# Optimization experiments

Measured on AMD Instinct MI355X. Metric: run time of the kernel, lower is better.

## Reference

```python
import jax, jax.numpy as jnp
import numpy as np

B, N, E = 8, 2000, 32000
LAT, STY, NF = 128, 64, 10
HEADS, HID = 4, 128
OUT = 3 + NF  # 13
EPS = 1e-5
SLOPE = 0.2


def _lin(k, fi, fo):
    return jax.random.normal(k, (fi, fo), dtype=jnp.float32) / np.sqrt(fi)


def setup_inputs() -> dict:
    key = jax.random.key(0)
    ks = jax.random.split(key, 32)
    inp = {
        'z': jax.random.normal(ks[0], (B, LAT), dtype=jnp.float32),
        'template_x': jax.random.normal(ks[1], (N, NF), dtype=jnp.float32),
        'template_edge_index': jax.random.randint(ks[2], (2, E), 0, N, dtype=jnp.int32),
        # style MLP
        'mlp_w1': _lin(ks[3], LAT, 256), 'mlp_b1': jnp.zeros((256,), jnp.float32),
        'mlp_w2': _lin(ks[4], 256, 512), 'mlp_b2': jnp.zeros((512,), jnp.float32),
        'mlp_w3': _lin(ks[5], 512, STY), 'mlp_b3': jnp.zeros((STY,), jnp.float32),
        # GAT1: in = NF + STY = 74 -> heads*HID = 512, concat
        'gat1_w': _lin(ks[6], NF + STY, HEADS * HID),
        'gat1_as': jax.random.normal(ks[7], (HEADS, HID), jnp.float32) * 0.1,
        'gat1_ad': jax.random.normal(ks[8], (HEADS, HID), jnp.float32) * 0.1,
        'gat1_b': jnp.zeros((HEADS * HID,), jnp.float32),
        'ln1_g': jnp.ones((HEADS * HID,), jnp.float32), 'ln1_b': jnp.zeros((HEADS * HID,), jnp.float32),
        # GAT2: 512 -> 512, concat
        'gat2_w': _lin(ks[9], HEADS * HID, HEADS * HID),
        'gat2_as': jax.random.normal(ks[10], (HEADS, HID), jnp.float32) * 0.1,
        'gat2_ad': jax.random.normal(ks[11], (HEADS, HID), jnp.float32) * 0.1,
        'gat2_b': jnp.zeros((HEADS * HID,), jnp.float32),
        'ln2_g': jnp.ones((HEADS * HID,), jnp.float32), 'ln2_b': jnp.zeros((HEADS * HID,), jnp.float32),
        # GAT3: 512 -> 13, 1 head, no concat
        'gat3_w': _lin(ks[12], HEADS * HID, OUT),
        'gat3_as': jax.random.normal(ks[13], (1, OUT), jnp.float32) * 0.1,
        'gat3_ad': jax.random.normal(ks[14], (1, OUT), jnp.float32) * 0.1,
        'gat3_b': jnp.zeros((OUT,), jnp.float32),
    }
    return inp


def gat_conv(x, src, dst, n_nodes, W, a_src, a_dst, bias, heads, out_ch, concat):
    # x: [NT, F_in]; per-head linear transform
    h = (x @ W).reshape(-1, heads, out_ch)              # [NT, H, C]
    als = jnp.sum(h * a_src[None], axis=-1)             # [NT, H]
    ald = jnp.sum(h * a_dst[None], axis=-1)             # [NT, H]
    logits = jax.nn.leaky_relu(als[src] + ald[dst], SLOPE)   # [E, H]
    # segment softmax over destination nodes (self-loops guarantee nonempty segments)
    mx = jax.ops.segment_max(logits, dst, num_segments=n_nodes)
    alpha = jnp.exp(logits - mx[dst])
    den = jax.ops.segment_sum(alpha, dst, num_segments=n_nodes)
    alpha = alpha / den[dst]                             # [E, H]
    msgs = h[src] * alpha[:, :, None]                    # [E, H, C]
    out = jax.ops.segment_sum(msgs, dst, num_segments=n_nodes)  # [NT, H, C]
    if concat:
        return out.reshape(n_nodes, heads * out_ch) + bias
    return out.mean(axis=1) + bias


def layer_norm(x, g, b):
    mu = jnp.mean(x, axis=-1, keepdims=True)
    var = jnp.mean((x - mu) ** 2, axis=-1, keepdims=True)
    return (x - mu) * jax.lax.rsqrt(var + EPS) * g + b


def reference(z, template_x, template_edge_index,
              mlp_w1, mlp_b1, mlp_w2, mlp_b2, mlp_w3, mlp_b3,
              gat1_w, gat1_as, gat1_ad, gat1_b, ln1_g, ln1_b,
              gat2_w, gat2_as, gat2_ad, gat2_b, ln2_g, ln2_b,
              gat3_w, gat3_as, gat3_ad, gat3_b):
    bsz = z.shape[0]
    n = template_x.shape[0]
    nt = bsz * n
    # batch the template graph: replicate nodes, offset edge indices per graph
    x = jnp.tile(template_x, (bsz, 1))                                  # [NT, NF]
    off = (jnp.arange(bsz, dtype=template_edge_index.dtype) * n)
    ei = (template_edge_index[:, None, :] + off[None, :, None]).reshape(2, -1)  # [2, B*E]
    loops = jnp.arange(nt, dtype=ei.dtype)
    src = jnp.concatenate([ei[0], loops])
    dst = jnp.concatenate([ei[1], loops])
    # style MLP
    s = jax.nn.leaky_relu(z @ mlp_w1 + mlp_b1, SLOPE)
    s = jax.nn.leaky_relu(s @ mlp_w2 + mlp_b2, SLOPE)
    s = s @ mlp_w3 + mlp_b3                                             # [B, STY]
    s_exp = jnp.repeat(s, n, axis=0)                                    # [NT, STY]
    H0 = jnp.concatenate([x, s_exp], axis=1)
    H1 = jax.nn.leaky_relu(gat_conv(H0, src, dst, nt, gat1_w, gat1_as, gat1_ad, gat1_b, HEADS, HID, True), SLOPE)
    H1n = layer_norm(H1, ln1_g, ln1_b)
    H2 = jax.nn.leaky_relu(gat_conv(H1n, src, dst, nt, gat2_w, gat2_as, gat2_ad, gat2_b, HEADS, HID, True), SLOPE)
    H2 = H2 + H1n
    H2n = layer_norm(H2, ln2_g, ln2_b)
    H_out = gat_conv(H2n, src, dst, nt, gat3_w, gat3_as, gat3_ad, gat3_b, 1, OUT, False)  # [NT, 13]
    delta_p = H_out[:, :3]
    delta_f = H_out[:, 3:]
    p_gen = x[:, :3] + delta_p
    X_gen = jnp.concatenate([p_gen, x[:, 3:] + delta_f[:, 3:]], axis=1)  # X[:, :3] overwritten by p_gen
    EF = p_gen[ei[1]] - p_gen[ei[0]]                                     # edge displacement vectors [B*E, 3]
    return X_gen, p_gen, EF
```

## Files before the change

kernel.cpp:

```cpp
#include <hip/hip_runtime.h>
#include <hip/hip_fp16.h>

constexpr int Bz = 8, Nn = 2000, Ee = 32000, NTOT = 16000;
constexpr int XG_OFF = 0, PG_OFF = 160000, EF_OFF = 208000;
#define SLOPE 0.2f
#define EPSL 1e-5f

typedef __attribute__((ext_vector_type(8))) _Float16 f16x8;
typedef __attribute__((ext_vector_type(4))) float float4v;

__device__ __forceinline__ float lrelu(float x) { return x > 0.f ? x : SLOPE * x; }

__device__ __forceinline__ unsigned short f2h(float x) {
  _Float16 hh = (_Float16)x;
  return *(unsigned short*)&hh;
}

__device__ __forceinline__ float wave_max(float v) {
  for (int o = 32; o; o >>= 1) v = fmaxf(v, __shfl_xor(v, o));
  return v;
}
__device__ __forceinline__ float wave_sum(float v) {
  for (int o = 32; o; o >>= 1) v += __shfl_xor(v, o);
  return v;
}

__global__ void hist_k(const int* __restrict__ tei, int* __restrict__ counts) {
  int j = blockIdx.x * 256 + threadIdx.x;
  if (j < Ee) atomicAdd(&counts[tei[Ee + j]], 1);
}

__global__ void scan_k(const int* __restrict__ counts, int* __restrict__ offs) {
  __shared__ int part[256];
  int t = threadIdx.x;
  int loc[8];
  int s = 0;
  for (int i = 0; i < 8; i++) {
    int idx = t * 8 + i;
    int c = (idx < Nn) ? counts[idx] : 0;
    loc[i] = s; s += c;
  }
  part[t] = s;
  __syncthreads();
  for (int o = 1; o < 256; o <<= 1) {
    int v = (t >= o) ? part[t - o] : 0;
    __syncthreads();
    part[t] += v;
    __syncthreads();
  }
  int excl = (t == 0) ? 0 : part[t - 1];
  for (int i = 0; i < 8; i++) {
    int idx = t * 8 + i;
    if (idx < Nn) offs[idx] = excl + loc[i];
  }
  if (t == 255) offs[Nn] = part[255];
}

__global__ void place_k(const int* __restrict__ tei, const int* __restrict__ offs,
                        int* __restrict__ cursor, int* __restrict__ colb) {
  int j = blockIdx.x * 256 + threadIdx.x;
  if (j < Ee) {
    int d = tei[Ee + j];
    int slot = offs[d] + atomicAdd(&cursor[d], 1);
    colb[slot] = tei[j];
  }
}

template <int K, int ACT>
__global__ __launch_bounds__(256) void lin_k(const float* __restrict__ x, const float* __restrict__ w,
                                             const float* __restrict__ bias, float* __restrict__ y,
                                             int O) {
  int gw = blockIdx.x * 4 + (threadIdx.x >> 6);
  int lane = threadIdx.x & 63;
  int bb = gw / O, o = gw - bb * O;
  float acc = 0.f;
#pragma unroll
  for (int k = lane; k < K; k += 64) acc += x[bb * K + k] * w[k * O + o];
  acc = wave_sum(acc);
  if (lane == 0) {
    if (bias) acc += bias[o];
    y[gw] = ACT ? lrelu(acc) : acc;
  }
}

__global__ __launch_bounds__(256) void w2bf_k(const float* __restrict__ W, unsigned short* __restrict__ Bt) {
  __shared__ float tile[32][33];
  int tx = threadIdx.x & 31, ty = threadIdx.x >> 5;
  int x0 = blockIdx.x * 32;
  int y0 = blockIdx.y * 32;
  for (int r = ty; r < 32; r += 8) tile[r][tx] = W[(y0 + r) * 512 + x0 + tx];
  __syncthreads();
  for (int r = ty; r < 32; r += 8) Bt[(x0 + r) * 512 + (y0 + tx)] = f2h(tile[tx][r]);
}

__global__ void w3t_k(const float* __restrict__ W, unsigned short* __restrict__ W3t) {
  for (int idx = threadIdx.x; idx < 8192; idx += 256) {
    int col = idx >> 9, k = idx & 511;
    float v = (col < 13) ? W[k * 13 + col] : 0.f;
    W3t[idx] = f2h(v);
  }
}

__global__ __launch_bounds__(256) void h1_k(const float* __restrict__ tx, const float* __restrict__ g1w,
                                            const float* __restrict__ pb,
                                            const float* __restrict__ a_s, const float* __restrict__ a_d,
                                            unsigned short* __restrict__ h1, float* __restrict__ als,
                                            float* __restrict__ ald) {
  int blk = blockIdx.x;
  int b = blk & 7, nl = blk >> 3;
  int n = b * Nn + nl;
  int head = threadIdx.x >> 6, lane = threadIdx.x & 63;
  int c = head * 128 + 2 * lane;
  float t0 = 0.f, t1 = 0.f;
#pragma unroll
  for (int k = 0; k < 10; k++) {
    float xv = tx[nl * 10 + k];
    float2 wv = *(const float2*)&g1w[k * 512 + c];
    t0 += xv * wv.x; t1 += xv * wv.y;
  }
  float2 pv = *(const float2*)&pb[b * 512 + c];
  float hx = t0 + pv.x, hy = t1 + pv.y;
  ushort2 st; st.x = f2h(hx); st.y = f2h(hy);
  *(ushort2*)&h1[(size_t)n * 512 + c] = st;
  float2 av = *(const float2*)&a_s[c];
  float2 dv = *(const float2*)&a_d[c];
  float pa = wave_sum(hx * av.x + hy * av.y);
  float pd = wave_sum(hx * dv.x + hy * dv.y);
  if (lane == 0) { als[n * 4 + head] = pa; ald[n * 4 + head] = pd; }
}

template <int RESID>
__global__ __launch_bounds__(256) void agg_k(const unsigned short* __restrict__ h,
                                             const float* __restrict__ als, const float* __restrict__ ald,
                                             const float* __restrict__ bias,
                                             const float* __restrict__ g, const float* __restrict__ beta,
                                             const unsigned short* __restrict__ resid,
                                             unsigned short* __restrict__ out,
                                             const int* __restrict__ offs, const int* __restrict__ colb) {
  int blk = blockIdx.x;
  int b = blk & 7, nl = blk >> 3;
  int n = b * Nn + nl;
  int w = threadIdx.x >> 6, lane = threadIdx.x & 63;
  int li = lane & 15, eg = lane >> 4;
  int rs = offs[nl];
  int nit = offs[nl + 1] - rs + 1;
  float aldn = ald[n * 4 + w];

  __shared__ float fin[512];
  __shared__ float red[8];
  __shared__ float bcs[2];

  __half2 acc2[4];
#pragma unroll
  for (int j = 0; j < 4; j++) acc2[j] = __float2half2_rn(0.f);
  float inv;
  const unsigned short* hbase = h + (size_t)(w * 128 + li * 8);

  if (nit <= 64) {
    int sg = n;
    float logit = -3e38f;
    if (lane < nit) {
      sg = (lane < nit - 1) ? colb[rs + lane] + b * Nn : n;
      logit = lrelu(als[sg * 4 + w] + aldn);
    }
    float m = wave_max(logit);
    float raw = (lane < nit) ? __expf(logit - m) : 0.f;
    inv = 1.f / wave_sum(raw);
    __half2 a2r = __float2half2_rn(raw);
    int au = *(int*)&a2r;
    for (int e = eg; e < nit; e += 4) {
      int aeu = __shfl(au, e);
      int sge = __shfl(sg, e);
      __half2 a2 = *(__half2*)&aeu;
      uint4 hv = *(const uint4*)(hbase + (size_t)sge * 512);
      acc2[0] = __hfma2(a2, *(__half2*)&hv.x, acc2[0]);
      acc2[1] = __hfma2(a2, *(__half2*)&hv.y, acc2[1]);
      acc2[2] = __hfma2(a2, *(__half2*)&hv.z, acc2[2]);
      acc2[3] = __hfma2(a2, *(__half2*)&hv.w, acc2[3]);
    }
  } else {
    float m = -3e38f;
    for (int i = lane; i < nit; i += 64) {
      int sg = (i < nit - 1) ? colb[rs + i] + b * Nn : n;
      m = fmaxf(m, lrelu(als[sg * 4 + w] + aldn));
    }
    m = wave_max(m);
    float den = 0.f;
    for (int base = 0; base < nit; base += 64) {
      int cnt = min(64, nit - base);
      int sg = n;
      float raw = 0.f;
      if (lane < cnt) {
        int i = base + lane;
        sg = (i < nit - 1) ? colb[rs + i] + b * Nn : n;
        raw = __expf(lrelu(als[sg * 4 + w] + aldn) - m);
      }
      den += raw;
      __half2 a2r = __float2half2_rn(raw);
      int au = *(int*)&a2r;
      for (int e = eg; e < cnt; e += 4) {
        int aeu = __shfl(au, e);
        int sge = __shfl(sg, e);
        __half2 a2 = *(__half2*)&aeu;
        uint4 hv = *(const uint4*)(hbase + (size_t)sge * 512);
        acc2[0] = __hfma2(a2, *(__half2*)&hv.x, acc2[0]);
        acc2[1] = __hfma2(a2, *(__half2*)&hv.y, acc2[1]);
        acc2[2] = __hfma2(a2, *(__half2*)&hv.z, acc2[2]);
        acc2[3] = __hfma2(a2, *(__half2*)&hv.w, acc2[3]);
      }
    }
    inv = 1.f / wave_sum(den);
  }

  float fv[8];
#pragma unroll
  for (int j = 0; j < 4; j++) {
    float2 f2 = __half22float2(acc2[j]);
    fv[2 * j] = f2.x; fv[2 * j + 1] = f2.y;
  }
#pragma unroll
  for (int j = 0; j < 8; j++) {
    fv[j] += __shfl_xor(fv[j], 16);
    fv[j] += __shfl_xor(fv[j], 32);
  }
  if (eg == 0) {
#pragma unroll
    for (int j = 0; j < 8; j++) fin[w * 128 + li * 8 + j] = fv[j] * inv;
  }
  __syncthreads();

  int c = 2 * threadIdx.x;
  float v0 = lrelu(fin[c] + bias[c]);
  float v1 = lrelu(fin[c + 1] + bias[c + 1]);
  if (RESID) {
    unsigned int rv = *(const unsigned int*)&resid[(size_t)n * 512 + c];
    __half2 rh = *(__half2*)&rv;
    float2 rf = __half22float2(rh);
    v0 += rf.x; v1 += rf.y;
  }
  float p1 = wave_sum(v0 + v1);
  float p2 = wave_sum(v0 * v0 + v1 * v1);
  if (lane == 0) { red[w] = p1; red[4 + w] = p2; }
  __syncthreads();
  if (threadIdx.x == 0) {
    float s1 = red[0] + red[1] + red[2] + red[3];
    float s2 = red[4] + red[5] + red[6] + red[7];
    float mu = s1 * (1.f / 512.f);
    float var = s2 * (1.f / 512.f) - mu * mu;
    bcs[0] = mu;
    bcs[1] = rsqrtf(var + EPSL);
  }
  __syncthreads();
  float mu = bcs[0], rstd = bcs[1];
  float o0 = (v0 - mu) * rstd * g[c] + beta[c];
  float o1 = (v1 - mu) * rstd * g[c + 1] + beta[c + 1];
  ushort2 st; st.x = f2h(o0); st.y = f2h(o1);
  *(ushort2*)&out[(size_t)n * 512 + c] = st;
}

__global__ __launch_bounds__(256) void gemm2_k(const unsigned short* __restrict__ A,
                                               const unsigned short* __restrict__ Bt,
                                               unsigned short* __restrict__ C,
                                               const float* __restrict__ As, const float* __restrict__ Ad,
                                               float* __restrict__ als2, float* __restrict__ ald2) {
  __shared__ char smem[32768];
  char* sAc = smem;
  char* sBc = smem + 16384;
  int t = threadIdx.x;
  int lane = t & 63, w = t >> 6;
  int wr = w >> 1, wc = w & 1;
  int m0 = blockIdx.y * 128, n0 = blockIdx.x * 128;
  int head = blockIdx.x;

  float4v acc[4][4];
#pragma unroll
  for (int i = 0; i < 4; i++)
#pragma unroll
    for (int j = 0; j < 4; j++) acc[i][j] = (float4v){0.f, 0.f, 0.f, 0.f};

  int srow[4], sklin[4], ssw[4];
#pragma unroll
  for (int i = 0; i < 4; i++) {
    int slot = i * 256 + t;
    srow[i] = slot >> 3;
    sklin[i] = (slot & 7) * 16;
    ssw[i] = srow[i] * 128 + (sklin[i] ^ ((srow[i] & 7) << 4));
  }

  uint4 va[4], vb[4];
#pragma unroll
  for (int i = 0; i < 4; i++) {
    va[i] = *(const uint4*)((const char*)A + (size_t)(m0 + srow[i]) * 1024 + sklin[i]);
    vb[i] = *(const uint4*)((const char*)Bt + (size_t)(n0 + srow[i]) * 1024 + sklin[i]);
  }

  int r_a = wr * 64 + (lane & 15);
  int r_b = wc * 64 + (lane & 15);
  int kbb = (lane >> 4) * 16;
  int sw_a = (r_a & 7) << 4;
  int sw_b = (r_b & 7) << 4;

  for (int k0 = 0; k0 < 512; k0 += 64) {
    if (k0) __syncthreads();
#pragma unroll
    for (int i = 0; i < 4; i++) {
      *(uint4*)(sAc + ssw[i]) = va[i];
      *(uint4*)(sBc + ssw[i]) = vb[i];
    }
    __syncthreads();
    if (k0 + 64 < 512) {
#pragma unroll
      for (int i = 0; i < 4; i++) {
        va[i] = *(const uint4*)((const char*)A + (size_t)(m0 + srow[i]) * 1024 + (k0 + 64) * 2 + sklin[i]);
        vb[i] = *(const uint4*)((const char*)Bt + (size_t)(n0 + srow[i]) * 1024 + (k0 + 64) * 2 + sklin[i]);
      }
    }
#pragma unroll
    for (int ksub = 0; ksub < 2; ksub++) {
      f16x8 af[4], bg[4];
#pragma unroll
      for (int m = 0; m < 4; m++)
        af[m] = *(const f16x8*)(sAc + (r_a + m * 16) * 128 + ((ksub * 64 + kbb) ^ sw_a));
#pragma unroll
      for (int nn = 0; nn < 4; nn++)
        bg[nn] = *(const f16x8*)(sBc + (r_b + nn * 16) * 128 + ((ksub * 64 + kbb) ^ sw_b));
#pragma unroll
      for (int m = 0; m < 4; m++)
#pragma unroll
        for (int nn = 0; nn < 4; nn++)
          acc[m][nn] = __builtin_amdgcn_mfma_f32_16x16x32_f16(af[m], bg[nn], acc[m][nn], 0, 0, 0);
    }
  }

  int orow = m0 + wr * 64 + (lane >> 4) * 4;
  int ocol = n0 + wc * 64 + (lane & 15);
#pragma unroll
  for (int m = 0; m < 4; m++)
#pragma unroll
    for (int nn = 0; nn < 4; nn++)
#pragma unroll
      for (int r = 0; r < 4; r++)
        C[(size_t)(orow + m * 16 + r) * 512 + ocol + nn * 16] = f2h(acc[m][nn][r]);

  __syncthreads();
  float* sRed = (float*)smem;
  int cidx0 = wc * 64 + (lane & 15);
  float asv[4], adv[4];
#pragma unroll
  for (int nn = 0; nn < 4; nn++) {
    asv[nn] = As[head * 128 + cidx0 + nn * 16];
    adv[nn] = Ad[head * 128 + cidx0 + nn * 16];
  }
#pragma unroll
  for (int m = 0; m < 4; m++) {
#pragma unroll
    for (int r = 0; r < 4; r++) {
      float pa = 0.f, pd = 0.f;
#pragma unroll
      for (int nn = 0; nn < 4; nn++) { pa += acc[m][nn][r] * asv[nn]; pd += acc[m][nn][r] * adv[nn]; }
      for (int o = 1; o < 16; o <<= 1) { pa += __shfl_xor(pa, o); pd += __shfl_xor(pd, o); }
      if ((lane & 15) == 0) {
        int rblk = wr * 64 + (lane >> 4) * 4 + m * 16 + r;
        sRed[rblk * 2 + wc] = pa;
        sRed[256 + rblk * 2 + wc] = pd;
      }
    }
  }
  __syncthreads();
  if (t < 128) {
    als2[(m0 + t) * 4 + head] = sRed[t * 2] + sRed[t * 2 + 1];
  } else {
    int r2 = t - 128;
    ald2[(m0 + r2) * 4 + head] = sRed[256 + r2 * 2] + sRed[256 + r2 * 2 + 1];
  }
}

__global__ __launch_bounds__(256) void gemm3_k(const unsigned short* __restrict__ H,
                                               const unsigned short* __restrict__ W3t,
                                               const float* __restrict__ as3, const float* __restrict__ ad3,
                                               float* __restrict__ h3, float* __restrict__ als3,
                                               float* __restrict__ ald3) {
  int w = threadIdx.x >> 6, l = threadIdx.x & 63;
  int m0 = blockIdx.x * 64 + w * 16;
  int r16 = l & 15, g4 = l >> 4;
  float4v acc = (float4v){0.f, 0.f, 0.f, 0.f};
  const unsigned short* ha = H + (size_t)(m0 + r16) * 512 + g4 * 8;
  const unsigned short* wb = W3t + (size_t)r16 * 512 + g4 * 8;
#pragma unroll
  for (int kk = 0; kk < 16; kk++) {
    f16x8 a = *(const f16x8*)(ha + kk * 32);
    f16x8 bfr = *(const f16x8*)(wb + kk * 32);
    acc = __builtin_amdgcn_mfma_f32_16x16x32_f16(a, bfr, acc, 0, 0, 0);
  }
  int col = r16;
  float asv = (col < 13) ? as3[col] : 0.f;
  float adv = (col < 13) ? ad3[col] : 0.f;
#pragma unroll
  for (int r = 0; r < 4; r++) {
    float v = acc[r];
    int row = m0 + g4 * 4 + r;
    if (col < 13) h3[row * 13 + col] = v;
    float sa = v * asv, sd = v * adv;
    for (int o = 1; o < 16; o <<= 1) { sa += __shfl_xor(sa, o); sd += __shfl_xor(sd, o); }
    if (col == 0) { als3[row] = sa; ald3[row] = sd; }
  }
}

__global__ __launch_bounds__(64) void agg3_k(const float* __restrict__ h3, const float* __restrict__ als3,
                                             const float* __restrict__ ald3, const float* __restrict__ b3,
                                             const float* __restrict__ tx, const int* __restrict__ offs,
                                             const int* __restrict__ colb, float* __restrict__ dout) {
  int blk = blockIdx.x, lane = threadIdx.x;
  int b = blk & 7, nl = blk >> 3;
  int n = b * Nn + nl;
  int rs = offs[nl], deg = offs[nl + 1] - rs;
  float aldn = ald3[n];
  float sl = lrelu(als3[n] + aldn);
  float a = 0.f, inv;
  if (deg <= 64) {
    int sgl = 0; float logit = -1e30f;
    if (lane < deg) { sgl = colb[rs + lane] + b * Nn; logit = lrelu(als3[sgl] + aldn); }
    float m = wave_max(fmaxf(logit, sl));
    float raw = (lane < deg) ? __expf(logit - m) : 0.f;
    float es = __expf(sl - m);
    inv = 1.f / (wave_sum(raw) + es);
    if (lane < 13) a = es * h3[n * 13 + lane];
    for (int e = 0; e < deg; e++) {
      float w = __shfl(raw, e);
      int sg = __shfl(sgl, e);
      if (lane < 13) a += w * h3[sg * 13 + lane];
    }
  } else {
    float m = sl;
    for (int e = lane; e < deg; e += 64) {
      int sg = colb[rs + e] + b * Nn;
      m = fmaxf(m, lrelu(als3[sg] + aldn));
    }
    m = wave_max(m);
    float es = __expf(sl - m);
    float den = (lane == 0) ? es : 0.f;
    if (lane < 13) a = es * h3[n * 13 + lane];
    for (int base = 0; base < deg; base += 64) {
      int cnt = min(64, deg - base);
      int sgl = 0; float raw = 0.f;
      if (lane < cnt) {
        sgl = colb[rs + base + lane] + b * Nn;
        raw = __expf(lrelu(als3[sgl] + aldn) - m);
      }
      den += raw;
      for (int e = 0; e < cnt; e++) {
        float w = __shfl(raw, e);
        int sg = __shfl(sgl, e);
        if (lane < 13) a += w * h3[sg * 13 + lane];
      }
    }
    inv = 1.f / wave_sum(den);
  }
  a *= inv;
  float hv = a + ((lane < 13) ? b3[lane] : 0.f);
  float txv = (lane < 10) ? tx[nl * 10 + lane] : 0.f;
  float pv = txv + hv;
  if (lane < 3) dout[PG_OFF + n * 3 + lane] = pv;
  float up = __shfl(hv, lane + 3);
  float xg = (lane < 3) ? pv : (txv + up);
  if (lane < 10) dout[XG_OFF + n * 10 + lane] = xg;
}

__global__ void ef_k(const int* __restrict__ tei, float* __restrict__ dout) {
  int e = blockIdx.x * 256 + threadIdx.x;
  int b = e / Ee, j = e - b * Ee;
  int sg = tei[j] + b * Nn;
  int dg = tei[Ee + j] + b * Nn;
  const float* pg = dout + PG_OFF;
  dout[EF_OFF + e * 3 + 0] = pg[dg * 3 + 0] - pg[sg * 3 + 0];
  dout[EF_OFF + e * 3 + 1] = pg[dg * 3 + 1] - pg[sg * 3 + 1];
  dout[EF_OFF + e * 3 + 2] = pg[dg * 3 + 2] - pg[sg * 3 + 2];
}

extern "C" void kernel_launch(void* const* d_in, const int* in_sizes, int n_in,
                              void* d_out, int out_size, void* d_ws, size_t ws_size,
                              hipStream_t stream) {
  const float* z = (const float*)d_in[0];
  const float* tx = (const float*)d_in[1];
  const int* tei = (const int*)d_in[2];
  const float* w1 = (const float*)d_in[3];
  const float* b1 = (const float*)d_in[4];
  const float* w2 = (const float*)d_in[5];
  const float* b2 = (const float*)d_in[6];
  const float* w3 = (const float*)d_in[7];
  const float* b3 = (const float*)d_in[8];
  const float* g1w = (const float*)d_in[9];
  const float* g1as = (const float*)d_in[10];
  const float* g1ad = (const float*)d_in[11];
  const float* g1b = (const float*)d_in[12];
  const float* ln1g = (const float*)d_in[13];
  const float* ln1b = (const float*)d_in[14];
  const float* g2w = (const float*)d_in[15];
  const float* g2as = (const float*)d_in[16];
  const float* g2ad = (const float*)d_in[17];
  const float* g2b = (const float*)d_in[18];
  const float* ln2g = (const float*)d_in[19];
  const float* ln2b = (const float*)d_in[20];
  const float* g3w = (const float*)d_in[21];
  const float* g3as = (const float*)d_in[22];
  const float* g3ad = (const float*)d_in[23];
  const float* g3b = (const float*)d_in[24];
  float* out = (float*)d_out;

  float* F = (float*)d_ws;
  float* pb_ = F + 0;
  float* l1_ = F + 8192;
  float* l2_ = F + 16384;
  float* s_ = F + 24576;
  float* als1 = F + 100000;
  float* ald1 = F + 164000;
  float* als2 = F + 228000;
  float* ald2 = F + 292000;
  float* als3 = F + 356000;
  float* ald3 = F + 372000;
  float* h3_ = F + 388000;
  unsigned short* U = (unsigned short*)(F + 600000);
  unsigned short* hA = U;
  unsigned short* hB = U + 8192000;
  unsigned short* Bt = U + 16384000;
  unsigned short* W3t = U + 16646144;
  int* I = (int*)(F + 10000000);
  int* counts = I;
  int* cursor = I + 2000;
  int* offs = I + 4000;
  int* colb = I + 6001;

  hipMemsetAsync(counts, 0, 4000 * sizeof(int), stream);
  hist_k<<<125, 256, 0, stream>>>(tei, counts);
  scan_k<<<1, 256, 0, stream>>>(counts, offs);
  place_k<<<125, 256, 0, stream>>>(tei, offs, cursor, colb);

  w2bf_k<<<dim3(16, 16), 256, 0, stream>>>(g2w, Bt);
  w3t_k<<<1, 256, 0, stream>>>(g3w, W3t);

  lin_k<128, 1><<<512, 256, 0, stream>>>(z, w1, b1, l1_, 256);
  lin_k<256, 1><<<1024, 256, 0, stream>>>(l1_, w2, b2, l2_, 512);
  lin_k<512, 0><<<128, 256, 0, stream>>>(l2_, w3, b3, s_, 64);
  lin_k<64, 0><<<1024, 256, 0, stream>>>(s_, g1w + 10 * 512, nullptr, pb_, 512);

  h1_k<<<NTOT, 256, 0, stream>>>(tx, g1w, pb_, g1as, g1ad, hA, als1, ald1);
  agg_k<0><<<NTOT, 256, 0, stream>>>(hA, als1, ald1, g1b, ln1g, ln1b, nullptr, hB, offs, colb);

  gemm2_k<<<dim3(4, 125), 256, 0, stream>>>(hB, Bt, hA, g2as, g2ad, als2, ald2);
  agg_k<1><<<NTOT, 256, 0, stream>>>(hA, als2, ald2, g2b, ln2g, ln2b, hB, hB, offs, colb);

  gemm3_k<<<250, 256, 0, stream>>>(hB, W3t, g3as, g3ad, h3_, als3, ald3);
  agg3_k<<<NTOT, 64, 0, stream>>>(h3_, als3, ald3, g3b, tx, offs, colb, out);
  ef_k<<<1000, 256, 0, stream>>>(tei, out);
}
```

Measured before the change: 235.2 us.

## Restructure GAT aggregation edge split and stage GEMM output through LDS

The aggregation kernel now splits edges across the four waves, with each lane covering 8 of the 512 features of a gathered row. Attention weights and source indices go through shared memory instead of wave shuffles, and per-wave partial sums are reduced in LDS before bias, residual and layernorm. This replaces 16-byte gathers from scattered lanes with full-row coalesced 1 KB reads, but adds block barriers and extra LDS traffic. The GEMM epilogue now stages its fp16 tile in padded shared memory and writes it out as 16-byte stores, replacing scattered 2-byte global stores.

```diff
diff --git a/kernel.cpp b/kernel.cpp
--- a/kernel.cpp
+++ b/kernel.cpp
@@ -141,20 +141,23 @@
   int b = blk & 7, nl = blk >> 3;
   int n = b * Nn + nl;
   int w = threadIdx.x >> 6, lane = threadIdx.x & 63;
-  int li = lane & 15, eg = lane >> 4;
   int rs = offs[nl];
   int nit = offs[nl + 1] - rs + 1;
   float aldn = ald[n * 4 + w];
 
-  __shared__ float fin[512];
+  __shared__ unsigned int alpha_u[4][68];
+  __shared__ int sgn[64];
+  __shared__ float part[4][512];
+  __shared__ float invs[4];
   __shared__ float red[8];
   __shared__ float bcs[2];
 
   __half2 acc2[4];
 #pragma unroll
   for (int j = 0; j < 4; j++) acc2[j] = __float2half2_rn(0.f);
-  float inv;
-  const unsigned short* hbase = h + (size_t)(w * 128 + li * 8);
+
+  const unsigned short* hbase = h + lane * 8;
+  int hd = lane >> 4;
 
   if (nit <= 64) {
     int sg = n;
@@ -162,21 +165,43 @@
     if (lane < nit) {
       sg = (lane < nit - 1) ? colb[rs + lane] + b * Nn : n;
       logit = lrelu(als[sg * 4 + w] + aldn);
+      if (w == 0) sgn[lane] = sg;
     }
     float m = wave_max(logit);
     float raw = (lane < nit) ? __expf(logit - m) : 0.f;
-    inv = 1.f / wave_sum(raw);
-    __half2 a2r = __float2half2_rn(raw);
-    int au = *(int*)&a2r;
-    for (int e = eg; e < nit; e += 4) {
-      int aeu = __shfl(au, e);
-      int sge = __shfl(sg, e);
-      __half2 a2 = *(__half2*)&aeu;
-      uint4 hv = *(const uint4*)(hbase + (size_t)sge * 512);
-      acc2[0] = __hfma2(a2, *(__half2*)&hv.x, acc2[0]);
-      acc2[1] = __hfma2(a2, *(__half2*)&hv.y, acc2[1]);
-      acc2[2] = __hfma2(a2, *(__half2*)&hv.z, acc2[2]);
-      acc2[3] = __hfma2(a2, *(__half2*)&hv.w, acc2[3]);
+    float den = wave_sum(raw);
+    if (lane == 0) invs[w] = 1.f / den;
+    __half2 a2 = __float2half2_rn(raw);
+    alpha_u[w][lane] = *(unsigned int*)&a2;
+    __syncthreads();
+    int e = w;
+    for (; e + 4 < nit; e += 8) {
+      unsigned int au0 = alpha_u[hd][e];
+      int sg0 = sgn[e];
+      unsigned int au1 = alpha_u[hd][e + 4];
+      int sg1 = sgn[e + 4];
+      uint4 hv0 = *(const uint4*)(hbase + (size_t)sg0 * 512);
+      uint4 hv1 = *(const uint4*)(hbase + (size_t)sg1 * 512);
+      __half2 a0 = *(__half2*)&au0;
+      __half2 a1 = *(__half2*)&au1;
+      acc2[0] = __hfma2(a0, *(__half2*)&hv0.x, acc2[0]);
+      acc2[1] = __hfma2(a0, *(__half2*)&hv0.y, acc2[1]);
+      acc2[2] = __hfma2(a0, *(__half2*)&hv0.z, acc2[2]);
+      acc2[3] = __hfma2(a0, *(__half2*)&hv0.w, acc2[3]);
+      acc2[0] = __hfma2(a1, *(__half2*)&hv1.x, acc2[0]);
+      acc2[1] = __hfma2(a1, *(__half2*)&hv1.y, acc2[1]);
+      acc2[2] = __hfma2(a1, *(__half2*)&hv1.z, acc2[2]);
+      acc2[3] = __hfma2(a1, *(__half2*)&hv1.w, acc2[3]);
+    }
+    if (e < nit) {
+      unsigned int au0 = alpha_u[hd][e];
+      int sg0 = sgn[e];
+      uint4 hv0 = *(const uint4*)(hbase + (size_t)sg0 * 512);
+      __half2 a0 = *(__half2*)&au0;
+      acc2[0] = __hfma2(a0, *(__half2*)&hv0.x, acc2[0]);
+      acc2[1] = __hfma2(a0, *(__half2*)&hv0.y, acc2[1]);
+      acc2[2] = __hfma2(a0, *(__half2*)&hv0.z, acc2[2]);
+      acc2[3] = __hfma2(a0, *(__half2*)&hv0.w, acc2[3]);
     }
   } else {
     float m = -3e38f;
@@ -194,22 +219,26 @@
         int i = base + lane;
         sg = (i < nit - 1) ? colb[rs + i] + b * Nn : n;
         raw = __expf(lrelu(als[sg * 4 + w] + aldn) - m);
+        if (w == 0) sgn[lane] = sg;
       }
       den += raw;
-      __half2 a2r = __float2half2_rn(raw);
-      int au = *(int*)&a2r;
-      for (int e = eg; e < cnt; e += 4) {
-        int aeu = __shfl(au, e);
-        int sge = __shfl(sg, e);
-        __half2 a2 = *(__half2*)&aeu;
+      __half2 a2 = __float2half2_rn(raw);
+      alpha_u[w][lane] = *(unsigned int*)&a2;
+      __syncthreads();
+      for (int e = w; e < cnt; e += 4) {
+        unsigned int au = alpha_u[hd][e];
+        int sge = sgn[e];
         uint4 hv = *(const uint4*)(hbase + (size_t)sge * 512);
-        acc2[0] = __hfma2(a2, *(__half2*)&hv.x, acc2[0]);
-        acc2[1] = __hfma2(a2, *(__half2*)&hv.y, acc2[1]);
-        acc2[2] = __hfma2(a2, *(__half2*)&hv.z, acc2[2]);
-        acc2[3] = __hfma2(a2, *(__half2*)&hv.w, acc2[3]);
+        __half2 a2e = *(__half2*)&au;
+        acc2[0] = __hfma2(a2e, *(__half2*)&hv.x, acc2[0]);
+        acc2[1] = __hfma2(a2e, *(__half2*)&hv.y, acc2[1]);
+        acc2[2] = __hfma2(a2e, *(__half2*)&hv.z, acc2[2]);
+        acc2[3] = __hfma2(a2e, *(__half2*)&hv.w, acc2[3]);
       }
-    }
-    inv = 1.f / wave_sum(den);
+      __syncthreads();
+    }
+    den = wave_sum(den);
+    if (lane == 0) invs[w] = 1.f / den;
   }
 
   float fv[8];
@@ -218,20 +247,16 @@
     float2 f2 = __half22float2(acc2[j]);
     fv[2 * j] = f2.x; fv[2 * j + 1] = f2.y;
   }
-#pragma unroll
-  for (int j = 0; j < 8; j++) {
-    fv[j] += __shfl_xor(fv[j], 16);
-    fv[j] += __shfl_xor(fv[j], 32);
-  }
-  if (eg == 0) {
-#pragma unroll
-    for (int j = 0; j < 8; j++) fin[w * 128 + li * 8 + j] = fv[j] * inv;
-  }
-  __syncthreads();
-
-  int c = 2 * threadIdx.x;
-  float v0 = lrelu(fin[c] + bias[c]);
-  float v1 = lrelu(fin[c + 1] + bias[c + 1]);
+  *(float4*)&part[w][lane * 8] = make_float4(fv[0], fv[1], fv[2], fv[3]);
+  *(float4*)&part[w][lane * 8 + 4] = make_float4(fv[4], fv[5], fv[6], fv[7]);
+  __syncthreads();
+
+  int c = 2 * (int)threadIdx.x;
+  float inv = invs[c >> 7];
+  float s0 = part[0][c] + part[1][c] + part[2][c] + part[3][c];
+  float s1 = part[0][c + 1] + part[1][c + 1] + part[2][c + 1] + part[3][c + 1];
+  float v0 = lrelu(s0 * inv + bias[c]);
+  float v1 = lrelu(s1 * inv + bias[c + 1]);
   if (RESID) {
     unsigned int rv = *(const unsigned int*)&resid[(size_t)n * 512 + c];
     __half2 rh = *(__half2*)&rv;
@@ -243,10 +268,10 @@
   if (lane == 0) { red[w] = p1; red[4 + w] = p2; }
   __syncthreads();
   if (threadIdx.x == 0) {
-    float s1 = red[0] + red[1] + red[2] + red[3];
-    float s2 = red[4] + red[5] + red[6] + red[7];
-    float mu = s1 * (1.f / 512.f);
-    float var = s2 * (1.f / 512.f) - mu * mu;
+    float s1r = red[0] + red[1] + red[2] + red[3];
+    float s2r = red[4] + red[5] + red[6] + red[7];
+    float mu = s1r * (1.f / 512.f);
+    float var = s2r * (1.f / 512.f) - mu * mu;
     bcs[0] = mu;
     bcs[1] = rsqrtf(var + EPSL);
   }
@@ -263,7 +288,7 @@
                                                unsigned short* __restrict__ C,
                                                const float* __restrict__ As, const float* __restrict__ Ad,
                                                float* __restrict__ als2, float* __restrict__ ald2) {
-  __shared__ char smem[32768];
+  __shared__ char smem[34816];
   char* sAc = smem;
   char* sBc = smem + 16384;
   int t = threadIdx.x;
@@ -332,15 +357,25 @@
     }
   }
 
-  int orow = m0 + wr * 64 + (lane >> 4) * 4;
-  int ocol = n0 + wc * 64 + (lane & 15);
+  __syncthreads();
+  unsigned short* sC = (unsigned short*)smem;
+  int rbase = wr * 64 + (lane >> 4) * 4;
+  int cbase = wc * 64 + (lane & 15);
 #pragma unroll
   for (int m = 0; m < 4; m++)
 #pragma unroll
     for (int nn = 0; nn < 4; nn++)
 #pragma unroll
       for (int r = 0; r < 4; r++)
-        C[(size_t)(orow + m * 16 + r) * 512 + ocol + nn * 16] = f2h(acc[m][nn][r]);
+        sC[(rbase + m * 16 + r) * 136 + cbase + nn * 16] = f2h(acc[m][nn][r]);
+  __syncthreads();
+#pragma unroll
+  for (int p = 0; p < 8; p++) {
+    int row = p * 16 + (t >> 4);
+    int co = (t & 15) * 8;
+    uint4 v = *(const uint4*)&sC[row * 136 + co];
+    *(uint4*)&C[(size_t)(m0 + row) * 512 + n0 + co] = v;
+  }
 
   __syncthreads();
   float* sRed = (float*)smem;
```

New measurement: 219.5 us. 1.07x faster.
